# Optimization experiments

Hardware: AMD Instinct MI355X
Metric: run time of the kernel (lower is better)

The kernel has to match this reference:

```python
import jax, jax.numpy as jnp
import numpy as np

NEG_SLOPE = 0.2


def add_self_loops(edge_index, num_nodes):
    loop = jnp.arange(num_nodes, dtype=edge_index.dtype)
    return jnp.concatenate([edge_index, jnp.stack([loop, loop])], axis=1)


def gat_conv(x, edge_index, W, att_src, att_dst, bias, heads, out_ch, concat):
    # x: [N, F_in]; edge_index: [2, E]; W: [F_in, heads*out_ch]
    # att_src/att_dst: [heads, out_ch]; bias: [heads*out_ch] or [out_ch]
    N = x.shape[0]
    ei = add_self_loops(edge_index, N)
    src, dst = ei[0], ei[1]
    xw = (x @ W).reshape(N, heads, out_ch)          # [N, H, C]
    a_src = jnp.einsum('nhc,hc->nh', xw, att_src)    # [N, H]
    a_dst = jnp.einsum('nhc,hc->nh', xw, att_dst)    # [N, H]
    e = a_src[src] + a_dst[dst]                      # [E', H]
    e = jax.nn.leaky_relu(e, NEG_SLOPE)
    # segment softmax over edges grouped by destination node
    e_max = jax.ops.segment_max(e, dst, num_segments=N)  # [N, H]
    e_exp = jnp.exp(e - e_max[dst])
    denom = jax.ops.segment_sum(e_exp, dst, num_segments=N)  # [N, H]
    alpha = e_exp / denom[dst]                       # [E', H]
    msg = xw[src] * alpha[:, :, None]                # [E', H, C]
    out = jax.ops.segment_sum(msg, dst, num_segments=N)  # [N, H, C]
    if concat:
        out = out.reshape(N, heads * out_ch)
    else:
        out = out.mean(axis=1)
    return out + bias


def setup_inputs() -> dict:
    key = jax.random.key(0)
    ks = jax.random.split(key, 10)
    N, E = 100000, 1600000
    F_in, hid, heads, F_out = 128, 32, 4, 40
    s = 0.1
    x = jax.random.normal(ks[0], (N, F_in), dtype=jnp.float32)
    edge_index = jax.random.randint(ks[1], (2, E), 0, N, dtype=jnp.int64)
    W1 = jax.random.normal(ks[2], (F_in, heads * hid), dtype=jnp.float32) * s
    att_src1 = jax.random.normal(ks[3], (heads, hid), dtype=jnp.float32) * s
    att_dst1 = jax.random.normal(ks[4], (heads, hid), dtype=jnp.float32) * s
    b1 = jax.random.normal(ks[5], (heads * hid,), dtype=jnp.float32) * s
    W2 = jax.random.normal(ks[6], (heads * hid, F_out), dtype=jnp.float32) * s
    att_src2 = jax.random.normal(ks[7], (1, F_out), dtype=jnp.float32) * s
    att_dst2 = jax.random.normal(ks[8], (1, F_out), dtype=jnp.float32) * s
    b2 = jax.random.normal(ks[9], (F_out,), dtype=jnp.float32) * s
    return {"x": x, "edge_index": edge_index, "W1": W1, "att_src1": att_src1,
            "att_dst1": att_dst1, "b1": b1, "W2": W2, "att_src2": att_src2,
            "att_dst2": att_dst2, "b2": b2}


def reference(x, edge_index, W1, att_src1, att_dst1, b1, W2, att_src2, att_dst2, b2):
    h = gat_conv(x, edge_index, W1, att_src1, att_dst1, b1, heads=4, out_ch=32, concat=True)
    h = jax.nn.relu(h)
    out = gat_conv(h, edge_index, W2, att_src2, att_dst2, b2, heads=1, out_ch=40, concat=True)
    return out
```

## Files before the change

kernel.cpp:

```cpp
#include <hip/hip_runtime.h>
#include <hip/hip_bf16.h>

#define NEG_SLOPE 0.2f
#define LOG2E 1.4426950408889634f
#define HWREG_XCC_ID_FULL (((32 - 1) << 11) | (0 << 6) | 20)

typedef _Float16 f16;
typedef f16 f16x8 __attribute__((ext_vector_type(8)));
typedef float f32x4 __attribute__((ext_vector_type(4)));

__device__ __forceinline__ float lrelu(float v) { return v > 0.f ? v : NEG_SLOPE * v; }

__device__ __forceinline__ unsigned pack_h2(float a, float b) {
    union { f16 h[2]; unsigned u; } c;
    c.h[0] = (f16)a; c.h[1] = (f16)b;
    return c.u;
}
__device__ __forceinline__ float2 unpack_h2(unsigned u) {
    union { unsigned u; f16 h[2]; } c;
    c.u = u;
    return make_float2((float)c.h[0], (float)c.h[1]);
}

__global__ void k_detect(const int* __restrict__ ei32, int npairs, int* flag) {
    __shared__ int found;
    if (threadIdx.x == 0) found = 0;
    __syncthreads();
    for (int i = threadIdx.x; i < npairs; i += blockDim.x) {
        if (ei32[2 * i + 1] != 0) found = 1;
    }
    __syncthreads();
    if (threadIdx.x == 0) *flag = found ? 0 : 1;
}

__device__ __forceinline__ void load_edge(const void* ei, int f64, int e, int E, int& s, int& d) {
    if (f64) {
        const long long* p = (const long long*)ei;
        s = (int)p[e];
        d = (int)p[(long long)E + e];
    } else {
        const int* p = (const int*)ei;
        s = p[e];
        d = p[E + e];
    }
}

__global__ void k_degree(const void* __restrict__ ei, const int* __restrict__ flag,
                         int* __restrict__ deg_part, int* __restrict__ rank, int N, int E) {
    int e = blockIdx.x * blockDim.x + threadIdx.x;
    if (e >= E) return;
    int s, d;
    load_edge(ei, *flag, e, E, s, d);
    int xcc = (int)(__builtin_amdgcn_s_getreg(HWREG_XCC_ID_FULL) & 7u);
    int lr = atomicAdd(&deg_part[xcc * N + d], 1);
    rank[e] = (xcc << 24) | lr;
}

__global__ void k_sumdeg(int* __restrict__ deg_part, int* __restrict__ deg, int N) {
    int d = blockIdx.x * blockDim.x + threadIdx.x;
    if (d >= N) return;
    int p = 0;
#pragma unroll
    for (int x = 0; x < 8; x++) {
        int t = deg_part[x * N + d];
        deg_part[x * N + d] = p;
        p += t;
    }
    deg[d] = p;
}

__global__ __launch_bounds__(1024) void k_scan_blk(const int* __restrict__ deg,
                                                   int* __restrict__ offsets,
                                                   int* __restrict__ blksum, int N) {
    __shared__ int wsums[16];
    const int t = threadIdx.x;
    const int lane = t & 63;
    const int wid = t >> 6;
    int idx = blockIdx.x * 4096 + t * 4;
    int v0 = (idx + 0 < N) ? deg[idx + 0] : 0;
    int v1 = (idx + 1 < N) ? deg[idx + 1] : 0;
    int v2 = (idx + 2 < N) ? deg[idx + 2] : 0;
    int v3 = (idx + 3 < N) ? deg[idx + 3] : 0;
    int s1 = v0 + v1, s2 = s1 + v2, s3 = s2 + v3;
    int inc = s3;
#pragma unroll
    for (int off = 1; off < 64; off <<= 1) {
        int y = __shfl_up(inc, off);
        if (lane >= off) inc += y;
    }
    if (lane == 63) wsums[wid] = inc;
    __syncthreads();
    if (wid == 0) {
        int v = (lane < 16) ? wsums[lane] : 0;
        int wi = v;
#pragma unroll
        for (int off = 1; off < 16; off <<= 1) {
            int y = __shfl_up(wi, off);
            if (lane >= off) wi += y;
        }
        if (lane < 16) wsums[lane] = wi - v;
        if (lane == 15) blksum[blockIdx.x] = wi;
    }
    __syncthreads();
    int excl = wsums[wid] + (inc - s3);
    if (idx + 0 < N) offsets[idx + 1] = excl + v0;
    if (idx + 1 < N) offsets[idx + 2] = excl + s1;
    if (idx + 2 < N) offsets[idx + 3] = excl + s2;
    if (idx + 3 < N) offsets[idx + 4] = excl + s3;
}

__global__ void k_scan_top(const int* __restrict__ blksum, int* __restrict__ blkoff, int G) {
    int l = threadIdx.x;
    int v = (l < G) ? blksum[l] : 0;
    int inc = v;
#pragma unroll
    for (int off = 1; off < 64; off <<= 1) {
        int y = __shfl_up(inc, off);
        if (l >= off) inc += y;
    }
    if (l < G) blkoff[l] = inc - v;
}

__global__ void k_scan_add(int* __restrict__ offsets, const int* __restrict__ blkoff, int N) {
    int n = blockIdx.x * blockDim.x + threadIdx.x;
    if (n >= N) return;
    offsets[n + 1] += blkoff[n >> 12];
    if (n == 0) offsets[0] = 0;
}

__global__ void k_scatter(const void* __restrict__ ei, const int* __restrict__ flag,
                          const int* __restrict__ offsets, const int* __restrict__ deg_part,
                          const int* __restrict__ rank, int* __restrict__ csr_src,
                          int N, int E) {
    int e = blockIdx.x * blockDim.x + threadIdx.x;
    if (e >= E) return;
    int s, d;
    load_edge(ei, *flag, e, E, s, d);
    int r = rank[e];
    int xcc = r >> 24;
    int lr = r & 0xFFFFFF;
    csr_src[offsets[d] + deg_part[xcc * N + d] + lr] = s;
}

__global__ void k_prep(const float* __restrict__ W1, const float* __restrict__ W2,
                       f16* __restrict__ W1t, f16* __restrict__ W2t) {
    int o = blockIdx.x * 256 + threadIdx.x;
    if (o < 128 * 128) {
        int n = o >> 7, k = o & 127;
        W1t[o] = (f16)W1[k * 128 + n];
    } else {
        int o2 = o - 128 * 128;
        if (o2 < 48 * 128) {
            int n = o2 >> 7, k = o2 & 127;
            W2t[o2] = (f16)(n < 40 ? W2[k * 40 + n] : 0.f);
        }
    }
}

__global__ __launch_bounds__(256) void k_gemm1(const float* __restrict__ X,
                                               const f16* __restrict__ W1t,
                                               f16* __restrict__ Af, int N) {
    __shared__ f16 sA[64 * 136];
    __shared__ f16 sB[128 * 136];
    const int t = threadIdx.x;
    const int row0 = blockIdx.x * 64;

    {
        int r = t >> 2, seg = t & 3;
        int row = row0 + r;
        if (row >= N) row = N - 1;
        const float4* xg = (const float4*)(X + (size_t)row * 128 + seg * 32);
        unsigned tmp[16];
#pragma unroll
        for (int j = 0; j < 8; j++) {
            float4 v = xg[j];
            tmp[2 * j]     = pack_h2(v.x, v.y);
            tmp[2 * j + 1] = pack_h2(v.z, v.w);
        }
        uint4* dst = (uint4*)&sA[r * 136 + seg * 32];
#pragma unroll
        for (int j = 0; j < 4; j++) dst[j] = ((uint4*)tmp)[j];
        int n = t >> 1, half = (t & 1) * 64;
        const uint4* src = (const uint4*)(W1t + n * 128 + half);
        uint4* dw = (uint4*)&sB[n * 136 + half];
#pragma unroll
        for (int j = 0; j < 8; j++) dw[j] = src[j];
    }
    __syncthreads();

    const int w = t >> 6, lane = t & 63, ln = lane & 15, q = lane >> 4;
    f32x4 acc[8];
#pragma unroll
    for (int c = 0; c < 8; c++) acc[c] = (f32x4){0.f, 0.f, 0.f, 0.f};

#pragma unroll
    for (int ks = 0; ks < 4; ks++) {
        f16x8 a = *(const f16x8*)&sA[(w * 16 + ln) * 136 + ks * 32 + q * 8];
#pragma unroll
        for (int c = 0; c < 8; c++) {
            f16x8 b = *(const f16x8*)&sB[(c * 16 + ln) * 136 + ks * 32 + q * 8];
            acc[c] = __builtin_amdgcn_mfma_f32_16x16x32_f16(a, b, acc[c], 0, 0, 0);
        }
    }

#pragma unroll
    for (int c = 0; c < 8; c++)
#pragma unroll
        for (int reg = 0; reg < 4; reg++) {
            int rg = row0 + w * 16 + q * 4 + reg;
            if (rg < N) Af[(size_t)rg * 128 + c * 16 + ln] = (f16)acc[c][reg];
        }
}

__global__ __launch_bounds__(256) void k_gemm2(const f16* __restrict__ Hf,
                                               const f16* __restrict__ W2t,
                                               f16* __restrict__ X2f, int N) {
    __shared__ f16 sA[64 * 136];
    __shared__ f16 sB[48 * 136];
    const int t = threadIdx.x;
    const int row0 = blockIdx.x * 64;
    {
        int r = t >> 2, seg = t & 3;
        int row = row0 + r;
        if (row >= N) row = N - 1;
        const uint4* hg = (const uint4*)(Hf + (size_t)row * 128 + seg * 32);
        uint4* dst = (uint4*)&sA[r * 136 + seg * 32];
#pragma unroll
        for (int j = 0; j < 4; j++) dst[j] = hg[j];
        const uint4* wsrc = (const uint4*)W2t;
#pragma unroll
        for (int u = t; u < 768; u += 256) {
            int o = u * 8;
            int n = o >> 7, ko = o & 127;
            *(uint4*)&sB[n * 136 + ko] = wsrc[u];
        }
    }
    __syncthreads();

    const int w = t >> 6, lane = t & 63, ln = lane & 15, q = lane >> 4;
    f32x4 acc[3];
#pragma unroll
    for (int c = 0; c < 3; c++) acc[c] = (f32x4){0.f, 0.f, 0.f, 0.f};

#pragma unroll
    for (int ks = 0; ks < 4; ks++) {
        f16x8 a = *(const f16x8*)&sA[(w * 16 + ln) * 136 + ks * 32 + q * 8];
#pragma unroll
        for (int c = 0; c < 3; c++) {
            f16x8 b = *(const f16x8*)&sB[(c * 16 + ln) * 136 + ks * 32 + q * 8];
            acc[c] = __builtin_amdgcn_mfma_f32_16x16x32_f16(a, b, acc[c], 0, 0, 0);
        }
    }

#pragma unroll
    for (int c = 0; c < 3; c++) {
        int col = c * 16 + ln;
        if (col < 40) {
#pragma unroll
            for (int reg = 0; reg < 4; reg++) {
                int rg = row0 + w * 16 + q * 4 + reg;
                if (rg < N) X2f[(size_t)rg * 40 + col] = (f16)acc[c][reg];
            }
        }
    }
}

__global__ void k_attn1(const f16* __restrict__ Af, const float* __restrict__ att_s,
                        const float* __restrict__ att_d, float* __restrict__ aS,
                        float* __restrict__ aD, int N) {
    int t = blockIdx.x * blockDim.x + threadIdx.x;
    if (t >= N * 4) return;
    int n = t >> 2, h = t & 3;
    const uint4* xr = (const uint4*)(Af + (size_t)n * 128 + h * 32);
    float ss = 0.f, sd = 0.f;
#pragma unroll
    for (int j = 0; j < 4; j++) {
        uint4 p = xr[j];
        float2 a0 = unpack_h2(p.x), a1 = unpack_h2(p.y), a2 = unpack_h2(p.z), a3 = unpack_h2(p.w);
        float xv[8] = {a0.x, a0.y, a1.x, a1.y, a2.x, a2.y, a3.x, a3.y};
        const float* as_ = att_s + h * 32 + j * 8;
        const float* ad_ = att_d + h * 32 + j * 8;
#pragma unroll
        for (int qq = 0; qq < 8; qq++) {
            ss += xv[qq] * as_[qq];
            sd += xv[qq] * ad_[qq];
        }
    }
    aS[t] = ss * LOG2E;
    aD[t] = sd * LOG2E;
}

__global__ void k_attn2(const f16* __restrict__ X2f, const float* __restrict__ att_s,
                        const float* __restrict__ att_d, float* __restrict__ aS,
                        float* __restrict__ aD, int N) {
    int n = blockIdx.x * blockDim.x + threadIdx.x;
    if (n >= N) return;
    const unsigned* xr = (const unsigned*)(X2f + (size_t)n * 40);
    float ss = 0.f, sd = 0.f;
#pragma unroll
    for (int j = 0; j < 20; j++) {
        float2 v = unpack_h2(xr[j]);
        ss += v.x * att_s[2 * j] + v.y * att_s[2 * j + 1];
        sd += v.x * att_d[2 * j] + v.y * att_d[2 * j + 1];
    }
    aS[n] = ss * LOG2E;
    aD[n] = sd * LOG2E;
}

__global__ __launch_bounds__(256) void k_msg1(const int* __restrict__ offsets,
                                              const int* __restrict__ csr_src,
                                              const float* __restrict__ aS,
                                              const float* __restrict__ aD,
                                              const f16* __restrict__ Af,
                                              const float* __restrict__ b1,
                                              f16* __restrict__ Hf, int N) {
    const int lane = threadIdx.x & 63;
    const int n = blockIdx.x * 4 + (threadIdx.x >> 6);
    const bool node_ok = (n < N);
    const int g = lane >> 4;
    const int p = lane & 15;
    const int h = p >> 2;

    int b = 0, e = 0;
    float adh = 0.f;
    if (node_ok) {
        b = offsets[n];
        e = offsets[n + 1];
        adh = aD[n * 4 + h];
    }

    float acc[8];
#pragma unroll
    for (int k = 0; k < 8; k++) acc[k] = 0.f;
    float wsum = 0.f;

    if (node_ok) {
        float xs = aS[n * 4 + h] + adh;
        float ws = __builtin_amdgcn_exp2f(fmaxf(xs, NEG_SLOPE * xs));
        if (g != 0) ws = 0.f;
        const f16x8 hv = *(const f16x8*)(Af + (size_t)n * 128 + p * 8);
#pragma unroll
        for (int k = 0; k < 8; k++) acc[k] = fmaf(ws, (float)hv[k], acc[k]);
        wsum = ws;
    }

    int sreg = 0;
    if (node_ok && e > b) {
        int idx = b + lane;
        if (idx >= e) idx = e - 1;
        sreg = csr_src[idx];
    }

    int i = b;
#pragma unroll 2
    for (; i < e && (i - b) + 4 <= 64; i += 4) {
        int j = i + g;
        bool valid = (j < e);
        int s = __builtin_amdgcn_ds_bpermute((j - b) << 2, sreg);
        if (!valid) s = 0;
        float sv = aS[s * 4 + h];
        const f16x8 hv = *(const f16x8*)(Af + (size_t)s * 128 + p * 8);
        float x = sv + adh;
        float wgt = __builtin_amdgcn_exp2f(fmaxf(x, NEG_SLOPE * x));
        if (!valid) wgt = 0.f;
#pragma unroll
        for (int k = 0; k < 8; k++) acc[k] = fmaf(wgt, (float)hv[k], acc[k]);
        wsum += wgt;
    }
    for (; i < e; i += 4) {
        int j = i + g;
        bool valid = (j < e);
        int jc = valid ? j : (e - 1);
        int s = csr_src[jc];
        if (!valid) s = 0;
        float sv = aS[s * 4 + h];
        const f16x8 hv = *(const f16x8*)(Af + (size_t)s * 128 + p * 8);
        float x = sv + adh;
        float wgt = __builtin_amdgcn_exp2f(fmaxf(x, NEG_SLOPE * x));
        if (!valid) wgt = 0.f;
#pragma unroll
        for (int k = 0; k < 8; k++) acc[k] = fmaf(wgt, (float)hv[k], acc[k]);
        wsum += wgt;
    }

#pragma unroll
    for (int k = 0; k < 8; k++) {
        acc[k] += __shfl_xor(acc[k], 16);
        acc[k] += __shfl_xor(acc[k], 32);
    }
    wsum += __shfl_xor(wsum, 16);
    wsum += __shfl_xor(wsum, 32);

    if (node_ok && g == 0) {
        float inv = __builtin_amdgcn_rcpf(wsum);
        const float4* bb = (const float4*)(b1 + p * 8);
        float4 b0 = bb[0], b4 = bb[1];
        float bv[8] = {b0.x, b0.y, b0.z, b0.w, b4.x, b4.y, b4.z, b4.w};
        union { f16 h8[8]; uint4 u; } o;
#pragma unroll
        for (int k = 0; k < 8; k++) {
            float v = fmaf(acc[k], inv, bv[k]);
            o.h8[k] = (f16)fmaxf(v, 0.f);
        }
        *(uint4*)(Hf + (size_t)n * 128 + p * 8) = o.u;
    }
}

__global__ __launch_bounds__(256) void k_msg2(const int* __restrict__ offsets,
                                              const int* __restrict__ csr_src,
                                              const float* __restrict__ aS,
                                              const float* __restrict__ aD,
                                              const f16* __restrict__ X2f,
                                              const float* __restrict__ b2,
                                              float* __restrict__ OUT, int N) {
    __shared__ float red[4][60][9];
    const int lane = threadIdx.x & 63;
    const int wv = threadIdx.x >> 6;
    const int n = blockIdx.x * 4 + wv;
    const bool node_ok = (n < N);
    const int g = lane / 5;
    const int p = lane % 5;
    const bool lane_ok = (g < 12);

    int b = 0, e = 0;
    float adh = 0.f;
    if (node_ok) {
        b = offsets[n];
        e = offsets[n + 1];
        adh = aD[n];
    }

    float acc[8];
#pragma unroll
    for (int k = 0; k < 8; k++) acc[k] = 0.f;
    float wsum = 0.f;

    if (node_ok) {
        float xs = aS[n] + adh;
        float ws = __builtin_amdgcn_exp2f(fmaxf(xs, NEG_SLOPE * xs));
        if (!(lane_ok && g == 0)) ws = 0.f;
        const f16x8 hv = *(const f16x8*)(X2f + (size_t)n * 40 + p * 8);
#pragma unroll
        for (int k = 0; k < 8; k++) acc[k] = fmaf(ws, (float)hv[k], acc[k]);
        wsum = ws;
    }

    int sreg = 0;
    if (node_ok && e > b) {
        int idx = b + lane;
        if (idx >= e) idx = e - 1;
        sreg = csr_src[idx];
    }

    int i = b;
    for (; i < e && (i - b) + 12 <= 64; i += 12) {
        int j = i + g;
        bool valid = lane_ok && (j < e);
        int s = __builtin_amdgcn_ds_bpermute(((j - b) & 63) << 2, sreg);
        if (!valid) s = 0;
        float sv = aS[s];
        const f16x8 hv = *(const f16x8*)(X2f + (size_t)s * 40 + p * 8);
        float x = sv + adh;
        float wgt = __builtin_amdgcn_exp2f(fmaxf(x, NEG_SLOPE * x));
        if (!valid) wgt = 0.f;
#pragma unroll
        for (int k = 0; k < 8; k++) acc[k] = fmaf(wgt, (float)hv[k], acc[k]);
        wsum += wgt;
    }
    for (; i < e; i += 12) {
        int j = i + g;
        bool valid = lane_ok && (j < e);
        int jc = (j < e) ? j : (e - 1);
        int s = csr_src[jc];
        if (!valid) s = 0;
        float sv = aS[s];
        const f16x8 hv = *(const f16x8*)(X2f + (size_t)s * 40 + p * 8);
        float x = sv + adh;
        float wgt = __builtin_amdgcn_exp2f(fmaxf(x, NEG_SLOPE * x));
        if (!valid) wgt = 0.f;
#pragma unroll
        for (int k = 0; k < 8; k++) acc[k] = fmaf(wgt, (float)hv[k], acc[k]);
        wsum += wgt;
    }

    if (lane_ok) {
#pragma unroll
        for (int k = 0; k < 8; k++) red[wv][lane][k] = acc[k];
        red[wv][lane][8] = wsum;
    }
    __syncthreads();

    if (node_ok && lane < 40) {
        int pp = lane >> 3, kk = lane & 7;
        float s_ = 0.f, ws_ = 0.f;
#pragma unroll
        for (int gg = 0; gg < 12; gg++) {
            s_  += red[wv][gg * 5 + pp][kk];
            ws_ += red[wv][gg * 5][8];
        }
        float inv = __builtin_amdgcn_rcpf(ws_);
        OUT[(size_t)n * 40 + lane] = fmaf(s_, inv, b2[lane]);
    }
}

extern "C" void kernel_launch(void* const* d_in, const int* in_sizes, int n_in,
                              void* d_out, int out_size, void* d_ws, size_t ws_size,
                              hipStream_t stream) {
    const float* x   = (const float*)d_in[0];
    const void*  ei  = d_in[1];
    const float* W1  = (const float*)d_in[2];
    const float* as1 = (const float*)d_in[3];
    const float* ad1 = (const float*)d_in[4];
    const float* b1  = (const float*)d_in[5];
    const float* W2  = (const float*)d_in[6];
    const float* as2 = (const float*)d_in[7];
    const float* ad2 = (const float*)d_in[8];
    const float* b2  = (const float*)d_in[9];
    float* out = (float*)d_out;

    const int N = in_sizes[0] / 128;
    const int E = in_sizes[1] / 2;

    char* w = (char*)d_ws;
    auto alloc = [&](size_t bytes) {
        char* p = w;
        w += (bytes + 15) & ~(size_t)15;
        return p;
    };
    int* flag      = (int*)alloc(16);
    int* offsets   = (int*)alloc((size_t)(N + 1) * 4);
    int* deg       = (int*)alloc((size_t)N * 4);
    int* deg_part  = (int*)alloc((size_t)N * 8 * 4);
    int* rank      = (int*)alloc((size_t)E * 4);
    int* csr_src   = (int*)alloc((size_t)E * 4);
    int* blksum    = (int*)alloc(64 * 4);
    int* blkoff    = (int*)alloc(64 * 4);
    float* aS1     = (float*)alloc((size_t)N * 4 * 4);
    float* aD1     = (float*)alloc((size_t)N * 4 * 4);
    float* aS2     = (float*)alloc((size_t)N * 4);
    float* aD2     = (float*)alloc((size_t)N * 4);
    f16* W1t       = (f16*)alloc(128 * 128 * 2);
    f16* W2t       = (f16*)alloc(48 * 128 * 2);
    f16* Af        = (f16*)alloc((size_t)N * 128 * 2);
    f16* X2f       = (f16*)alloc((size_t)N * 40 * 2);
    f16* Hf        = (f16*)alloc((size_t)N * 128 * 2);

    k_detect<<<1, 256, 0, stream>>>((const int*)ei, 1024, flag);
    k_prep<<<88, 256, 0, stream>>>(W1, W2, W1t, W2t);

    hipMemsetAsync(deg_part, 0, (size_t)N * 8 * 4, stream);
    k_degree<<<(E + 255) / 256, 256, 0, stream>>>(ei, flag, deg_part, rank, N, E);
    k_sumdeg<<<(N + 255) / 256, 256, 0, stream>>>(deg_part, deg, N);
    const int G = (N + 4095) / 4096;
    k_scan_blk<<<G, 1024, 0, stream>>>(deg, offsets, blksum, N);
    k_scan_top<<<1, 64, 0, stream>>>(blksum, blkoff, G);
    k_scan_add<<<(N + 255) / 256, 256, 0, stream>>>(offsets, blkoff, N);
    k_scatter<<<(E + 255) / 256, 256, 0, stream>>>(ei, flag, offsets, deg_part, rank,
                                                   csr_src, N, E);

    const int gb = (N + 63) / 64;
    k_gemm1<<<gb, 256, 0, stream>>>(x, W1t, Af, N);
    k_attn1<<<(N * 4 + 255) / 256, 256, 0, stream>>>(Af, as1, ad1, aS1, aD1, N);
    k_msg1<<<(N + 3) / 4, 256, 0, stream>>>(offsets, csr_src, aS1, aD1, Af, b1, Hf, N);

    k_gemm2<<<gb, 256, 0, stream>>>(Hf, W2t, X2f, N);
    k_attn2<<<(N + 255) / 256, 256, 0, stream>>>(X2f, as2, ad2, aS2, aD2, N);
    k_msg2<<<(N + 3) / 4, 256, 0, stream>>>(offsets, csr_src, aS2, aD2, X2f, b2, out, N);
}
```

Baseline: 390.8 us.

## Fuse attention-score dot products into GEMM epilogues and shrink message-passing blocks

Computes the per-node source/destination attention logits directly from the MFMA accumulators in the GEMM epilogues, using cross-lane shuffle reductions, and removes the separate k_attn1/k_attn2 kernels along with their re-read of the f16 features. The layer-2 feature row stride is padded from 40 to 64 halves so rows are better aligned for gathers, at the cost of more memory footprint. The message kernels now use 128-thread blocks holding two nodes each, and the k_msg1 edge loop is unrolled by four instead of two. The extra epilogue work adds register pressure and shuffles to the GEMMs.

```diff
diff --git a/kernel.cpp b/kernel.cpp
--- a/kernel.cpp
+++ b/kernel.cpp
@@ -8,18 +8,11 @@
 typedef _Float16 f16;
 typedef f16 f16x8 __attribute__((ext_vector_type(8)));
 typedef float f32x4 __attribute__((ext_vector_type(4)));
-
-__device__ __forceinline__ float lrelu(float v) { return v > 0.f ? v : NEG_SLOPE * v; }
 
 __device__ __forceinline__ unsigned pack_h2(float a, float b) {
     union { f16 h[2]; unsigned u; } c;
     c.h[0] = (f16)a; c.h[1] = (f16)b;
     return c.u;
-}
-__device__ __forceinline__ float2 unpack_h2(unsigned u) {
-    union { unsigned u; f16 h[2]; } c;
-    c.u = u;
-    return make_float2((float)c.h[0], (float)c.h[1]);
 }
 
 __global__ void k_detect(const int* __restrict__ ei32, int npairs, int* flag) {
@@ -159,7 +152,11 @@
 
 __global__ __launch_bounds__(256) void k_gemm1(const float* __restrict__ X,
                                                const f16* __restrict__ W1t,
-                                               f16* __restrict__ Af, int N) {
+                                               const float* __restrict__ as1,
+                                               const float* __restrict__ ad1,
+                                               f16* __restrict__ Af,
+                                               float* __restrict__ aS1,
+                                               float* __restrict__ aD1, int N) {
     __shared__ f16 sA[64 * 136];
     __shared__ f16 sB[128 * 136];
     const int t = threadIdx.x;
@@ -210,11 +207,53 @@
             int rg = row0 + w * 16 + q * 4 + reg;
             if (rg < N) Af[(size_t)rg * 128 + c * 16 + ln] = (f16)acc[c][reg];
         }
+
+    float ps[4][4], pd[4][4];
+#pragma unroll
+    for (int h = 0; h < 4; h++) {
+        float as_lo = as1[32 * h + ln], as_hi = as1[32 * h + 16 + ln];
+        float ad_lo = ad1[32 * h + ln], ad_hi = ad1[32 * h + 16 + ln];
+#pragma unroll
+        for (int reg = 0; reg < 4; reg++) {
+            ps[h][reg] = acc[2 * h][reg] * as_lo + acc[2 * h + 1][reg] * as_hi;
+            pd[h][reg] = acc[2 * h][reg] * ad_lo + acc[2 * h + 1][reg] * ad_hi;
+        }
+    }
+#pragma unroll
+    for (int h = 0; h < 4; h++)
+#pragma unroll
+        for (int reg = 0; reg < 4; reg++)
+#pragma unroll
+            for (int off = 1; off < 16; off <<= 1) {
+                ps[h][reg] += __shfl_xor(ps[h][reg], off);
+                pd[h][reg] += __shfl_xor(pd[h][reg], off);
+            }
+#pragma unroll
+    for (int h = 0; h < 4; h++) {
+        if (ln == 2 * h) {
+#pragma unroll
+            for (int reg = 0; reg < 4; reg++) {
+                int rg = row0 + w * 16 + q * 4 + reg;
+                if (rg < N) aS1[rg * 4 + h] = ps[h][reg] * LOG2E;
+            }
+        }
+        if (ln == 2 * h + 1) {
+#pragma unroll
+            for (int reg = 0; reg < 4; reg++) {
+                int rg = row0 + w * 16 + q * 4 + reg;
+                if (rg < N) aD1[rg * 4 + h] = pd[h][reg] * LOG2E;
+            }
+        }
+    }
 }
 
 __global__ __launch_bounds__(256) void k_gemm2(const f16* __restrict__ Hf,
                                                const f16* __restrict__ W2t,
-                                               f16* __restrict__ X2f, int N) {
+                                               const float* __restrict__ as2,
+                                               const float* __restrict__ ad2,
+                                               f16* __restrict__ X2f,
+                                               float* __restrict__ aS2,
+                                               float* __restrict__ aD2, int N) {
     __shared__ f16 sA[64 * 136];
     __shared__ f16 sB[48 * 136];
     const int t = threadIdx.x;
@@ -259,55 +298,41 @@
 #pragma unroll
             for (int reg = 0; reg < 4; reg++) {
                 int rg = row0 + w * 16 + q * 4 + reg;
-                if (rg < N) X2f[(size_t)rg * 40 + col] = (f16)acc[c][reg];
+                if (rg < N) X2f[(size_t)rg * 64 + col] = (f16)acc[c][reg];
             }
         }
     }
-}
-
-__global__ void k_attn1(const f16* __restrict__ Af, const float* __restrict__ att_s,
-                        const float* __restrict__ att_d, float* __restrict__ aS,
-                        float* __restrict__ aD, int N) {
-    int t = blockIdx.x * blockDim.x + threadIdx.x;
-    if (t >= N * 4) return;
-    int n = t >> 2, h = t & 3;
-    const uint4* xr = (const uint4*)(Af + (size_t)n * 128 + h * 32);
-    float ss = 0.f, sd = 0.f;
-#pragma unroll
-    for (int j = 0; j < 4; j++) {
-        uint4 p = xr[j];
-        float2 a0 = unpack_h2(p.x), a1 = unpack_h2(p.y), a2 = unpack_h2(p.z), a3 = unpack_h2(p.w);
-        float xv[8] = {a0.x, a0.y, a1.x, a1.y, a2.x, a2.y, a3.x, a3.y};
-        const float* as_ = att_s + h * 32 + j * 8;
-        const float* ad_ = att_d + h * 32 + j * 8;
-#pragma unroll
-        for (int qq = 0; qq < 8; qq++) {
-            ss += xv[qq] * as_[qq];
-            sd += xv[qq] * ad_[qq];
-        }
-    }
-    aS[t] = ss * LOG2E;
-    aD[t] = sd * LOG2E;
-}
-
-__global__ void k_attn2(const f16* __restrict__ X2f, const float* __restrict__ att_s,
-                        const float* __restrict__ att_d, float* __restrict__ aS,
-                        float* __restrict__ aD, int N) {
-    int n = blockIdx.x * blockDim.x + threadIdx.x;
-    if (n >= N) return;
-    const unsigned* xr = (const unsigned*)(X2f + (size_t)n * 40);
-    float ss = 0.f, sd = 0.f;
-#pragma unroll
-    for (int j = 0; j < 20; j++) {
-        float2 v = unpack_h2(xr[j]);
-        ss += v.x * att_s[2 * j] + v.y * att_s[2 * j + 1];
-        sd += v.x * att_d[2 * j] + v.y * att_d[2 * j + 1];
-    }
-    aS[n] = ss * LOG2E;
-    aD[n] = sd * LOG2E;
-}
-
-__global__ __launch_bounds__(256) void k_msg1(const int* __restrict__ offsets,
+
+    float ps[4], pd[4];
+#pragma unroll
+    for (int reg = 0; reg < 4; reg++) { ps[reg] = 0.f; pd[reg] = 0.f; }
+#pragma unroll
+    for (int c = 0; c < 3; c++) {
+        int col = c * 16 + ln;
+        float as_ = (col < 40) ? as2[col] : 0.f;
+        float ad_ = (col < 40) ? ad2[col] : 0.f;
+#pragma unroll
+        for (int reg = 0; reg < 4; reg++) {
+            ps[reg] = fmaf(acc[c][reg], as_, ps[reg]);
+            pd[reg] = fmaf(acc[c][reg], ad_, pd[reg]);
+        }
+    }
+#pragma unroll
+    for (int reg = 0; reg < 4; reg++) {
+#pragma unroll
+        for (int off = 1; off < 16; off <<= 1) {
+            ps[reg] += __shfl_xor(ps[reg], off);
+            pd[reg] += __shfl_xor(pd[reg], off);
+        }
+        int rg = row0 + w * 16 + q * 4 + reg;
+        if (rg < N) {
+            if (ln == 0) aS2[rg] = ps[reg] * LOG2E;
+            if (ln == 1) aD2[rg] = pd[reg] * LOG2E;
+        }
+    }
+}
+
+__global__ __launch_bounds__(128) void k_msg1(const int* __restrict__ offsets,
                                               const int* __restrict__ csr_src,
                                               const float* __restrict__ aS,
                                               const float* __restrict__ aD,
@@ -315,7 +340,7 @@
                                               const float* __restrict__ b1,
                                               f16* __restrict__ Hf, int N) {
     const int lane = threadIdx.x & 63;
-    const int n = blockIdx.x * 4 + (threadIdx.x >> 6);
+    const int n = blockIdx.x * 2 + (threadIdx.x >> 6);
     const bool node_ok = (n < N);
     const int g = lane >> 4;
     const int p = lane & 15;
@@ -352,7 +377,7 @@
     }
 
     int i = b;
-#pragma unroll 2
+#pragma unroll 4
     for (; i < e && (i - b) + 4 <= 64; i += 4) {
         int j = i + g;
         bool valid = (j < e);
@@ -406,17 +431,17 @@
     }
 }
 
-__global__ __launch_bounds__(256) void k_msg2(const int* __restrict__ offsets,
+__global__ __launch_bounds__(128) void k_msg2(const int* __restrict__ offsets,
                                               const int* __restrict__ csr_src,
                                               const float* __restrict__ aS,
                                               const float* __restrict__ aD,
                                               const f16* __restrict__ X2f,
                                               const float* __restrict__ b2,
                                               float* __restrict__ OUT, int N) {
-    __shared__ float red[4][60][9];
+    __shared__ float red[2][60][9];
     const int lane = threadIdx.x & 63;
     const int wv = threadIdx.x >> 6;
-    const int n = blockIdx.x * 4 + wv;
+    const int n = blockIdx.x * 2 + wv;
     const bool node_ok = (n < N);
     const int g = lane / 5;
     const int p = lane % 5;
@@ -439,7 +464,7 @@
         float xs = aS[n] + adh;
         float ws = __builtin_amdgcn_exp2f(fmaxf(xs, NEG_SLOPE * xs));
         if (!(lane_ok && g == 0)) ws = 0.f;
-        const f16x8 hv = *(const f16x8*)(X2f + (size_t)n * 40 + p * 8);
+        const f16x8 hv = *(const f16x8*)(X2f + (size_t)n * 64 + p * 8);
 #pragma unroll
         for (int k = 0; k < 8; k++) acc[k] = fmaf(ws, (float)hv[k], acc[k]);
         wsum = ws;
@@ -459,7 +484,7 @@
         int s = __builtin_amdgcn_ds_bpermute(((j - b) & 63) << 2, sreg);
         if (!valid) s = 0;
         float sv = aS[s];
-        const f16x8 hv = *(const f16x8*)(X2f + (size_t)s * 40 + p * 8);
+        const f16x8 hv = *(const f16x8*)(X2f + (size_t)s * 64 + p * 8);
         float x = sv + adh;
         float wgt = __builtin_amdgcn_exp2f(fmaxf(x, NEG_SLOPE * x));
         if (!valid) wgt = 0.f;
@@ -474,7 +499,7 @@
         int s = csr_src[jc];
         if (!valid) s = 0;
         float sv = aS[s];
-        const f16x8 hv = *(const f16x8*)(X2f + (size_t)s * 40 + p * 8);
+        const f16x8 hv = *(const f16x8*)(X2f + (size_t)s * 64 + p * 8);
         float x = sv + adh;
         float wgt = __builtin_amdgcn_exp2f(fmaxf(x, NEG_SLOPE * x));
         if (!valid) wgt = 0.f;
@@ -542,7 +567,7 @@
     f16* W1t       = (f16*)alloc(128 * 128 * 2);
     f16* W2t       = (f16*)alloc(48 * 128 * 2);
     f16* Af        = (f16*)alloc((size_t)N * 128 * 2);
-    f16* X2f       = (f16*)alloc((size_t)N * 40 * 2);
+    f16* X2f       = (f16*)alloc((size_t)N * 64 * 2);
     f16* Hf        = (f16*)alloc((size_t)N * 128 * 2);
 
     k_detect<<<1, 256, 0, stream>>>((const int*)ei, 1024, flag);
@@ -559,11 +584,9 @@
                                                    csr_src, N, E);
 
     const int gb = (N + 63) / 64;
-    k_gemm1<<<gb, 256, 0, stream>>>(x, W1t, Af, N);
-    k_attn1<<<(N * 4 + 255) / 256, 256, 0, stream>>>(Af, as1, ad1, aS1, aD1, N);
-    k_msg1<<<(N + 3) / 4, 256, 0, stream>>>(offsets, csr_src, aS1, aD1, Af, b1, Hf, N);
-
-    k_gemm2<<<gb, 256, 0, stream>>>(Hf, W2t, X2f, N);
-    k_attn2<<<(N + 255) / 256, 256, 0, stream>>>(X2f, as2, ad2, aS2, aD2, N);
-    k_msg2<<<(N + 3) / 4, 256, 0, stream>>>(offsets, csr_src, aS2, aD2, X2f, b2, out, N);
-}
+    k_gemm1<<<gb, 256, 0, stream>>>(x, W1t, as1, ad1, Af, aS1, aD1, N);
+    k_msg1<<<(N + 1) / 2, 128, 0, stream>>>(offsets, csr_src, aS1, aD1, Af, b1, Hf, N);
+
+    k_gemm2<<<gb, 256, 0, stream>>>(Hf, W2t, as2, ad2, X2f, aS2, aD2, N);
+    k_msg2<<<(N + 1) / 2, 128, 0, stream>>>(offsets, csr_src, aS2, aD2, X2f, b2, out, N);
+}
```

Result: no change. 388.3 us (-0.7%).
